# Optimization experiments

Measured on AMD Instinct MI355X. Metric: run time of the kernel, lower is better.

Reference implementation:

```python
import jax, jax.numpy as jnp
import numpy as np

N_NODES = 100000
N_EDGES = 1600000
D_FEAT = 64
HIDDEN = 64


def _glorot(key, shape):
    fan_in, fan_out = shape[1], shape[0]
    limit = float(np.sqrt(6.0 / (fan_in + fan_out)))
    return jax.random.uniform(key, shape, jnp.float32, -limit, limit)


def setup_inputs() -> dict:
    key = jax.random.key(0)
    ks = jax.random.split(key, 8)
    x = jax.random.normal(ks[0], (N_NODES, D_FEAT), jnp.float32)
    edge_index = jax.random.randint(ks[1], (2, N_EDGES), 0, N_NODES, jnp.int64)
    # SAGEConv params: lin_l applied to aggregated neighbors (has bias),
    # lin_r applied to root/self features (no bias in PyG default).
    params = {
        "W1_l": _glorot(ks[2], (HIDDEN, D_FEAT)),
        "b1": jnp.zeros((HIDDEN,), jnp.float32),
        "W1_r": _glorot(ks[3], (HIDDEN, D_FEAT)),
        "W2_l": _glorot(ks[4], (HIDDEN, HIDDEN)),
        "b2": jnp.zeros((HIDDEN,), jnp.float32),
        "W2_r": _glorot(ks[5], (HIDDEN, HIDDEN)),
    }
    return {"x": x, "edge_index": edge_index, **params}


def _sage_conv(x, src, dst, deg_inv, W_l, b, W_r):
    # mean-aggregate neighbor features: gather at src, segment-sum at dst
    msg = jax.ops.segment_sum(x[src], dst, num_segments=N_NODES)  # [N, F]
    agg = msg * deg_inv[:, None]
    return agg @ W_l.T + b + x @ W_r.T


def reference(x, edge_index, W1_l, b1, W1_r, W2_l, b2, W2_r):
    src, dst = edge_index[0], edge_index[1]
    deg = jax.ops.segment_sum(jnp.ones((N_EDGES,), x.dtype), dst,
                              num_segments=N_NODES)
    deg_inv = 1.0 / jnp.maximum(deg, 1.0)  # PyG mean clamps count to >=1
    h = jax.nn.relu(_sage_conv(x, src, dst, deg_inv, W1_l, b1, W1_r))
    out = _sage_conv(h, src, dst, deg_inv, W2_l, b2, W2_r)
    return out
```

## Files before the change

kernel.cpp:

```cpp
#include <hip/hip_runtime.h>
#include <hip/hip_bf16.h>

#define FEAT 64

typedef __bf16 bf16x8 __attribute__((ext_vector_type(8)));
typedef __bf16 bf16x4 __attribute__((ext_vector_type(4)));
typedef float  f32x4  __attribute__((ext_vector_type(4)));

__global__ __launch_bounds__(256)
void zero1_kernel(int* __restrict__ a, int n) {
    int i = blockIdx.x * 256 + threadIdx.x;
    if (i < n) a[i] = 0;
}

__global__ __launch_bounds__(256)
void zero2_kernel(int* __restrict__ a, int* __restrict__ b, int n) {
    int i = blockIdx.x * 256 + threadIdx.x;
    if (i < n) { a[i] = 0; b[i] = 0; }
}

__global__ void detect_idx_kernel(const unsigned* __restrict__ w, int* __restrict__ flag) {
    __shared__ int any_nz;
    if (threadIdx.x == 0) any_nz = 0;
    __syncthreads();
    if (w[2 * threadIdx.x + 1] != 0u) atomicOr(&any_nz, 1);
    __syncthreads();
    if (threadIdx.x == 0) *flag = (any_nz == 0) ? 1 : 0;
}

__device__ __forceinline__ int load_idx_clamped(const void* ei, long long i, int is64, int n_nodes) {
    int v = is64 ? (int)((const long long*)ei)[i] : ((const int*)ei)[i];
    v = v < 0 ? 0 : v;
    return v >= n_nodes ? n_nodes - 1 : v;
}


__global__ __launch_bounds__(256)
void bucket_count_kernel(const void* __restrict__ ei, const int* __restrict__ flagp,
                         int* __restrict__ gcnt, int n_edges, int n_nodes) {
    __shared__ int cnt[512];
    const int t = threadIdx.x;
    cnt[t] = 0; cnt[t + 256] = 0;
    __syncthreads();
    const int is64 = *flagp;
    for (int e = blockIdx.x * 256 + t; e < n_edges; e += gridDim.x * 256) {
        int d = load_idx_clamped(ei, (long long)n_edges + e, is64, n_nodes);
        atomicAdd(&cnt[d >> 9], 1);
    }
    __syncthreads();
    if (cnt[t])       atomicAdd(&gcnt[t], cnt[t]);
    if (cnt[t + 256]) atomicAdd(&gcnt[t + 256], cnt[t + 256]);
}

__global__ void bucket_scan_kernel(const int* __restrict__ gcnt, int* __restrict__ gbase,
                                   int* __restrict__ gcur, int n_edges) {
    __shared__ int sh[512];
    int t = threadIdx.x;
    int v = gcnt[t];
    sh[t] = v;
    __syncthreads();
    for (int off = 1; off < 512; off <<= 1) {
        int u = (t >= off) ? sh[t - off] : 0;
        __syncthreads();
        sh[t] += u;
        __syncthreads();
    }
    int excl = sh[t] - v;
    gbase[t] = excl;
    gcur[t]  = excl;
    if (t == 511) gbase[512] = n_edges;
}

__global__ __launch_bounds__(256)
void multisplit_kernel(const void* __restrict__ ei, const int* __restrict__ flagp,
                       int* __restrict__ gcur, unsigned* __restrict__ B,
                       int n_edges, int n_nodes) {
    __shared__ unsigned sv[4096];
    __shared__ unsigned dv[4096];
    __shared__ int cnt[512];
    __shared__ int cur[512];
    const int t = threadIdx.x;
    const int is64 = *flagp;
    const int ntiles = (n_edges + 4095) >> 12;
    for (int tile = blockIdx.x; tile < ntiles; tile += gridDim.x) {
        cnt[t] = 0; cnt[t + 256] = 0;
        __syncthreads();
        #pragma unroll
        for (int k = 0; k < 16; ++k) {
            int i = k * 256 + t;
            int e = (tile << 12) + i;
            unsigned dmark = 0xFFFFFFFFu, s = 0;
            if (e < n_edges) {
                s     = (unsigned)load_idx_clamped(ei, e, is64, n_nodes);
                int d = load_idx_clamped(ei, (long long)n_edges + e, is64, n_nodes);
                dmark = (unsigned)d;
                atomicAdd(&cnt[d >> 9], 1);
            }
            sv[i] = s; dv[i] = dmark;
        }
        __syncthreads();
        if (cnt[t])       cur[t]       = atomicAdd(&gcur[t], cnt[t]);
        if (cnt[t + 256]) cur[t + 256] = atomicAdd(&gcur[t + 256], cnt[t + 256]);
        __syncthreads();
        #pragma unroll
        for (int k = 0; k < 16; ++k) {
            int i = k * 256 + t;
            unsigned d = dv[i];
            if (d != 0xFFFFFFFFu) {
                int pos = atomicAdd(&cur[d >> 9], 1);
                pos = pos < 0 ? 0 : (pos >= n_edges ? n_edges - 1 : pos);
                B[pos] = ((d & 511u) << 17) | sv[i];
            }
        }
        __syncthreads();
    }
}

__global__ __launch_bounds__(256)
void csr_build2_kernel(const unsigned* __restrict__ B, const int* __restrict__ gbase,
                       int* __restrict__ degc, int* __restrict__ offs,
                       float* __restrict__ dinv, int* __restrict__ csr,
                       int n_edges, int n_nodes) {
    __shared__ int cnt[512];
    __shared__ int scn[512];
    __shared__ int cur[512];
    const int b = blockIdx.x, t = threadIdx.x;
    cnt[t] = 0; cnt[t + 256] = 0;
    __syncthreads();
    const int lo = gbase[b], hi = gbase[b + 1];
    for (int i = lo + t; i < hi; i += 256) {
        unsigned v = B[i];
        atomicAdd(&cnt[v >> 17], 1);
    }
    __syncthreads();
    scn[t] = cnt[t]; scn[t + 256] = cnt[t + 256];
    __syncthreads();
    for (int off = 1; off < 512; off <<= 1) {
        int u0 = (t >= off) ? scn[t - off] : 0;
        int u1 = (t + 256 >= off) ? scn[t + 256 - off] : 0;
        __syncthreads();
        scn[t] += u0; scn[t + 256] += u1;
        __syncthreads();
    }
    const int base = gbase[b];
    int e0 = base + scn[t] - cnt[t];
    int e1 = base + scn[t + 256] - cnt[t + 256];
    cur[t] = e0; cur[t + 256] = e1;
    int n0 = b * 512 + t, n1 = n0 + 256;
    if (n0 < n_nodes) {
        degc[n0] = cnt[t]; offs[n0] = e0;
        dinv[n0] = 1.0f / fmaxf((float)cnt[t], 1.0f);
    }
    if (n1 < n_nodes) {
        degc[n1] = cnt[t + 256]; offs[n1] = e1;
        dinv[n1] = 1.0f / fmaxf((float)cnt[t + 256], 1.0f);
    }
    __syncthreads();
    for (int i = lo + t; i < hi; i += 256) {
        unsigned v = B[i];
        int pos = atomicAdd(&cur[v >> 17], 1);
        pos = pos < 0 ? 0 : (pos >= n_edges ? n_edges - 1 : pos);
        csr[pos] = (int)(v & 0x1FFFFu);
    }
}

__global__ __launch_bounds__(256)
void scan_partial_kernel(const int* __restrict__ degc, int* __restrict__ part, int n_nodes) {
    __shared__ int sh[256];
    int i = blockIdx.x * 256 + threadIdx.x;
    sh[threadIdx.x] = (i < n_nodes) ? degc[i] : 0;
    __syncthreads();
    for (int off = 128; off > 0; off >>= 1) {
        if (threadIdx.x < off) sh[threadIdx.x] += sh[threadIdx.x + off];
        __syncthreads();
    }
    if (threadIdx.x == 0) part[blockIdx.x] = sh[0];
}

__global__ void scan_top_kernel(int* __restrict__ part, int nparts) {
    __shared__ int sh[512];
    int t = threadIdx.x;
    int v = (t < nparts) ? part[t] : 0;
    sh[t] = v;
    __syncthreads();
    for (int off = 1; off < 512; off <<= 1) {
        int u = (t >= off) ? sh[t - off] : 0;
        __syncthreads();
        sh[t] += u;
        __syncthreads();
    }
    if (t < nparts) part[t] = sh[t] - v;
}

__global__ __launch_bounds__(256)
void scan_final_kernel(const int* __restrict__ degc, const int* __restrict__ part,
                       int* __restrict__ offs, float* __restrict__ deg_inv, int n_nodes) {
    __shared__ int sh[256];
    int t = threadIdx.x;
    int i = blockIdx.x * 256 + t;
    int v = (i < n_nodes) ? degc[i] : 0;
    sh[t] = v;
    __syncthreads();
    for (int off = 1; off < 256; off <<= 1) {
        int u = (t >= off) ? sh[t - off] : 0;
        __syncthreads();
        sh[t] += u;
        __syncthreads();
    }
    if (i < n_nodes) {
        offs[i]    = sh[t] - v + part[blockIdx.x];
        deg_inv[i] = 1.0f / fmaxf((float)v, 1.0f);
    }
}

__global__ __launch_bounds__(256)
void hist_kernel(const void* __restrict__ ei, const int* __restrict__ flagp,
                 int* __restrict__ degc, int n_edges, int n_nodes) {
    int e = blockIdx.x * 256 + threadIdx.x;
    if (e >= n_edges) return;
    int d = load_idx_clamped(ei, (long long)n_edges + e, *flagp, n_nodes);
    atomicAdd(&degc[d], 1);
}

__global__ __launch_bounds__(256)
void csr_scatter_kernel(const void* __restrict__ ei, const int* __restrict__ flagp,
                        const int* __restrict__ offs, int* __restrict__ cursor,
                        int* __restrict__ csr, int n_edges, int n_nodes) {
    int e = blockIdx.x * 256 + threadIdx.x;
    if (e >= n_edges) return;
    int is64 = *flagp;
    int s = load_idx_clamped(ei, e, is64, n_nodes);
    int d = load_idx_clamped(ei, (long long)n_edges + e, is64, n_nodes);
    int pos = offs[d] + atomicAdd(&cursor[d], 1);
    pos = pos < 0 ? 0 : (pos >= n_edges ? n_edges - 1 : pos);
    csr[pos] = s;
}

__global__ __launch_bounds__(256)
void cast_w_kernel(const float* __restrict__ a, const float* __restrict__ b,
                   const float* __restrict__ c, const float* __restrict__ d,
                   __bf16* __restrict__ o) {
    int i = blockIdx.x * 256 + threadIdx.x;
    if (i < FEAT * FEAT) {
        o[i]         = (__bf16)a[i];
        o[4096 + i]  = (__bf16)b[i];
        o[8192 + i]  = (__bf16)c[i];
        o[12288 + i] = (__bf16)d[i];
    }
}

__global__ __launch_bounds__(256)
void cast_x_kernel(const float* __restrict__ x, __bf16* __restrict__ xb, int n4) {
    int i = blockIdx.x * 256 + threadIdx.x;
    if (i < n4) {
        float4 v = ((const float4*)x)[i];
        bf16x4 o;
        o.x = (__bf16)v.x; o.y = (__bf16)v.y; o.z = (__bf16)v.z; o.w = (__bf16)v.w;
        ((bf16x4*)xb)[i] = o;
    }
}

__global__ __launch_bounds__(256)
void gather_bf16_kernel(const __bf16* __restrict__ hin, const int* __restrict__ offs,
                        const int* __restrict__ degc, const float* __restrict__ dinv,
                        const int* __restrict__ csr, __bf16* __restrict__ agg,
                        int n_nodes) {
    const int t = threadIdx.x, lane = t & 63, g = lane >> 4, u = lane & 15;
    const int gw = blockIdx.x * 4 + (t >> 6), nw = gridDim.x * 4;
    for (int n = gw; n < n_nodes; n += nw) {
        int rs = offs[n], cnt = degc[n];
        float a0 = 0.f, a1 = 0.f, a2 = 0.f, a3 = 0.f;
        for (int c = 0; c < cnt; c += 64) {
            int chunk = min(64, cnt - c);
            int myid = (lane < chunk) ? (int)__builtin_nontemporal_load(&csr[rs + c + lane]) : 0;
            myid = myid < 0 ? 0 : (myid >= n_nodes ? n_nodes - 1 : myid);
            for (int q = 0; q < chunk; q += 16) {
                int q0 = q + g, q1 = q + g + 4, q2 = q + g + 8, q3 = q + g + 12;
                int s0 = __shfl(myid, q0);
                int s1 = __shfl(myid, q1);
                int s2 = __shfl(myid, q2);
                int s3 = __shfl(myid, q3);
                float m0 = (q0 < chunk) ? 1.f : 0.f;
                float m1 = (q1 < chunk) ? 1.f : 0.f;
                float m2 = (q2 < chunk) ? 1.f : 0.f;
                float m3 = (q3 < chunk) ? 1.f : 0.f;
                bf16x4 v0 = ((const bf16x4*)hin)[(size_t)s0 * 16 + u];
                bf16x4 v1 = ((const bf16x4*)hin)[(size_t)s1 * 16 + u];
                bf16x4 v2 = ((const bf16x4*)hin)[(size_t)s2 * 16 + u];
                bf16x4 v3 = ((const bf16x4*)hin)[(size_t)s3 * 16 + u];
                a0 = fmaf(m0, (float)v0.x, a0); a1 = fmaf(m0, (float)v0.y, a1);
                a2 = fmaf(m0, (float)v0.z, a2); a3 = fmaf(m0, (float)v0.w, a3);
                a0 = fmaf(m1, (float)v1.x, a0); a1 = fmaf(m1, (float)v1.y, a1);
                a2 = fmaf(m1, (float)v1.z, a2); a3 = fmaf(m1, (float)v1.w, a3);
                a0 = fmaf(m2, (float)v2.x, a0); a1 = fmaf(m2, (float)v2.y, a1);
                a2 = fmaf(m2, (float)v2.z, a2); a3 = fmaf(m2, (float)v2.w, a3);
                a0 = fmaf(m3, (float)v3.x, a0); a1 = fmaf(m3, (float)v3.y, a1);
                a2 = fmaf(m3, (float)v3.z, a2); a3 = fmaf(m3, (float)v3.w, a3);
            }
        }
        a0 += __shfl_xor(a0, 16); a1 += __shfl_xor(a1, 16);
        a2 += __shfl_xor(a2, 16); a3 += __shfl_xor(a3, 16);
        a0 += __shfl_xor(a0, 32); a1 += __shfl_xor(a1, 32);
        a2 += __shfl_xor(a2, 32); a3 += __shfl_xor(a3, 32);
        if (g == 0) {
            float di = dinv[n];
            bf16x4 o;
            o.x = (__bf16)(a0 * di); o.y = (__bf16)(a1 * di);
            o.z = (__bf16)(a2 * di); o.w = (__bf16)(a3 * di);
            ((bf16x4*)agg)[(size_t)n * 16 + u] = o;
        }
    }
}

__global__ __launch_bounds__(256)
void gather_f32_kernel(const float* __restrict__ xin, const int* __restrict__ offs,
                       const int* __restrict__ degc, const float* __restrict__ dinv,
                       const int* __restrict__ csr, __bf16* __restrict__ agg,
                       int n_nodes) {
    const int t = threadIdx.x, lane = t & 63, g = lane >> 4, u = lane & 15;
    const int gw = blockIdx.x * 4 + (t >> 6), nw = gridDim.x * 4;
    for (int n = gw; n < n_nodes; n += nw) {
        int rs = offs[n], cnt = degc[n];
        float a0 = 0.f, a1 = 0.f, a2 = 0.f, a3 = 0.f;
        for (int c = 0; c < cnt; c += 64) {
            int chunk = min(64, cnt - c);
            int myid = (lane < chunk) ? (int)__builtin_nontemporal_load(&csr[rs + c + lane]) : 0;
            myid = myid < 0 ? 0 : (myid >= n_nodes ? n_nodes - 1 : myid);
            for (int q = 0; q < chunk; q += 16) {
                int q0 = q + g, q1 = q + g + 4, q2 = q + g + 8, q3 = q + g + 12;
                int s0 = __shfl(myid, q0), s1 = __shfl(myid, q1);
                int s2 = __shfl(myid, q2), s3 = __shfl(myid, q3);
                float m0 = (q0 < chunk) ? 1.f : 0.f;
                float m1 = (q1 < chunk) ? 1.f : 0.f;
                float m2 = (q2 < chunk) ? 1.f : 0.f;
                float m3 = (q3 < chunk) ? 1.f : 0.f;
                float4 v0 = ((const float4*)xin)[(size_t)s0 * 16 + u];
                float4 v1 = ((const float4*)xin)[(size_t)s1 * 16 + u];
                float4 v2 = ((const float4*)xin)[(size_t)s2 * 16 + u];
                float4 v3 = ((const float4*)xin)[(size_t)s3 * 16 + u];
                a0 = fmaf(m0, v0.x, a0); a1 = fmaf(m0, v0.y, a1);
                a2 = fmaf(m0, v0.z, a2); a3 = fmaf(m0, v0.w, a3);
                a0 = fmaf(m1, v1.x, a0); a1 = fmaf(m1, v1.y, a1);
                a2 = fmaf(m1, v1.z, a2); a3 = fmaf(m1, v1.w, a3);
                a0 = fmaf(m2, v2.x, a0); a1 = fmaf(m2, v2.y, a1);
                a2 = fmaf(m2, v2.z, a2); a3 = fmaf(m2, v2.w, a3);
                a0 = fmaf(m3, v3.x, a0); a1 = fmaf(m3, v3.y, a1);
                a2 = fmaf(m3, v3.z, a2); a3 = fmaf(m3, v3.w, a3);
            }
        }
        a0 += __shfl_xor(a0, 16); a1 += __shfl_xor(a1, 16);
        a2 += __shfl_xor(a2, 16); a3 += __shfl_xor(a3, 16);
        a0 += __shfl_xor(a0, 32); a1 += __shfl_xor(a1, 32);
        a2 += __shfl_xor(a2, 32); a3 += __shfl_xor(a3, 32);
        if (g == 0) {
            float di = dinv[n];
            bf16x4 o;
            o.x = (__bf16)(a0 * di); o.y = (__bf16)(a1 * di);
            o.z = (__bf16)(a2 * di); o.w = (__bf16)(a3 * di);
            ((bf16x4*)agg)[(size_t)n * 16 + u] = o;
        }
    }
}

__global__ __launch_bounds__(256)
void gemm_l1b_kernel(const __bf16* __restrict__ Ag, const __bf16* __restrict__ xb,
                     const __bf16* __restrict__ Bl, const __bf16* __restrict__ Br,
                     const float* __restrict__ bias,
                     __bf16* __restrict__ hout, int n_nodes) {
    const int t = threadIdx.x, lane = t & 63;
    const int quad = lane >> 4, r16 = lane & 15;
    bf16x8 bl[2][4], br[2][4];
    #pragma unroll
    for (int ks = 0; ks < 2; ++ks)
        #pragma unroll
        for (int ct = 0; ct < 4; ++ct) {
            int f = ct * 16 + r16, k = ks * 32 + quad * 8;
            bl[ks][ct] = *(const bf16x8*)(Bl + f * 64 + k);
            br[ks][ct] = *(const bf16x8*)(Br + f * 64 + k);
        }
    const int m0 = (blockIdx.x * 4 + (t >> 6)) * 16;
    if (m0 >= n_nodes) return;
    int mrow = m0 + r16; if (mrow >= n_nodes) mrow = n_nodes - 1;
    bf16x8 ag[2], ax[2];
    #pragma unroll
    for (int ks = 0; ks < 2; ++ks) {
        ag[ks] = *(const bf16x8*)(Ag + (size_t)mrow * 64 + ks * 32 + quad * 8);
        ax[ks] = *(const bf16x8*)(xb + (size_t)mrow * 64 + ks * 32 + quad * 8);
    }
    #pragma unroll
    for (int ct = 0; ct < 4; ++ct) {
        f32x4 acc = {0.f, 0.f, 0.f, 0.f};
        acc = __builtin_amdgcn_mfma_f32_16x16x32_bf16(ag[0], bl[0][ct], acc, 0, 0, 0);
        acc = __builtin_amdgcn_mfma_f32_16x16x32_bf16(ag[1], bl[1][ct], acc, 0, 0, 0);
        acc = __builtin_amdgcn_mfma_f32_16x16x32_bf16(ax[0], br[0][ct], acc, 0, 0, 0);
        acc = __builtin_amdgcn_mfma_f32_16x16x32_bf16(ax[1], br[1][ct], acc, 0, 0, 0);
        int col = ct * 16 + r16;
        float bv = bias[col];
        #pragma unroll
        for (int rg = 0; rg < 4; ++rg) {
            int n = m0 + quad * 4 + rg;
            if (n < n_nodes) {
                float o = acc[rg] + bv;
                hout[(size_t)n * 64 + col] = (__bf16)fmaxf(o, 0.f);
            }
        }
    }
}

__global__ __launch_bounds__(256)
void gemm_l1_kernel(const __bf16* __restrict__ Ag, const float* __restrict__ xin,
                    const __bf16* __restrict__ Bl, const __bf16* __restrict__ Br,
                    const float* __restrict__ bias,
                    __bf16* __restrict__ hout, int n_nodes) {
    const int t = threadIdx.x, lane = t & 63;
    const int quad = lane >> 4, r16 = lane & 15;
    bf16x8 bl[2][4], br[2][4];
    #pragma unroll
    for (int ks = 0; ks < 2; ++ks)
        #pragma unroll
        for (int ct = 0; ct < 4; ++ct) {
            int f = ct * 16 + r16, k = ks * 32 + quad * 8;
            bl[ks][ct] = *(const bf16x8*)(Bl + f * 64 + k);
            br[ks][ct] = *(const bf16x8*)(Br + f * 64 + k);
        }
    const int m0 = (blockIdx.x * 4 + (t >> 6)) * 16;
    if (m0 >= n_nodes) return;
    int mrow = m0 + r16; if (mrow >= n_nodes) mrow = n_nodes - 1;
    bf16x8 ag[2], ax[2];
    #pragma unroll
    for (int ks = 0; ks < 2; ++ks) {
        ag[ks] = *(const bf16x8*)(Ag + (size_t)mrow * 64 + ks * 32 + quad * 8);
        const float* xr = xin + (size_t)mrow * 64 + ks * 32 + quad * 8;
        float4 p = *(const float4*)xr;
        float4 q = *(const float4*)(xr + 4);
        union { bf16x8 v; __bf16 e[8]; } U;
        U.e[0] = (__bf16)p.x; U.e[1] = (__bf16)p.y; U.e[2] = (__bf16)p.z; U.e[3] = (__bf16)p.w;
        U.e[4] = (__bf16)q.x; U.e[5] = (__bf16)q.y; U.e[6] = (__bf16)q.z; U.e[7] = (__bf16)q.w;
        ax[ks] = U.v;
    }
    #pragma unroll
    for (int ct = 0; ct < 4; ++ct) {
        f32x4 acc = {0.f, 0.f, 0.f, 0.f};
        acc = __builtin_amdgcn_mfma_f32_16x16x32_bf16(ag[0], bl[0][ct], acc, 0, 0, 0);
        acc = __builtin_amdgcn_mfma_f32_16x16x32_bf16(ag[1], bl[1][ct], acc, 0, 0, 0);
        acc = __builtin_amdgcn_mfma_f32_16x16x32_bf16(ax[0], br[0][ct], acc, 0, 0, 0);
        acc = __builtin_amdgcn_mfma_f32_16x16x32_bf16(ax[1], br[1][ct], acc, 0, 0, 0);
        int col = ct * 16 + r16;
        float bv = bias[col];
        #pragma unroll
        for (int rg = 0; rg < 4; ++rg) {
            int n = m0 + quad * 4 + rg;
            if (n < n_nodes) {
                float o = acc[rg] + bv;
                hout[(size_t)n * 64 + col] = (__bf16)fmaxf(o, 0.f);
            }
        }
    }
}

__global__ __launch_bounds__(256)
void gemm_l2_kernel(const __bf16* __restrict__ Ag, const __bf16* __restrict__ Ah,
                    const __bf16* __restrict__ Bl, const __bf16* __restrict__ Br,
                    const float* __restrict__ bias,
                    float* __restrict__ out, int n_nodes) {
    const int t = threadIdx.x, lane = t & 63;
    const int quad = lane >> 4, r16 = lane & 15;
    bf16x8 bl[2][4], br[2][4];
    #pragma unroll
    for (int ks = 0; ks < 2; ++ks)
        #pragma unroll
        for (int ct = 0; ct < 4; ++ct) {
            int f = ct * 16 + r16, k = ks * 32 + quad * 8;
            bl[ks][ct] = *(const bf16x8*)(Bl + f * 64 + k);
            br[ks][ct] = *(const bf16x8*)(Br + f * 64 + k);
        }
    const int m0 = (blockIdx.x * 4 + (t >> 6)) * 16;
    if (m0 >= n_nodes) return;
    int mrow = m0 + r16; if (mrow >= n_nodes) mrow = n_nodes - 1;
    bf16x8 ag[2], ah[2];
    #pragma unroll
    for (int ks = 0; ks < 2; ++ks) {
        ag[ks] = *(const bf16x8*)(Ag + (size_t)mrow * 64 + ks * 32 + quad * 8);
        ah[ks] = *(const bf16x8*)(Ah + (size_t)mrow * 64 + ks * 32 + quad * 8);
    }
    #pragma unroll
    for (int ct = 0; ct < 4; ++ct) {
        f32x4 acc = {0.f, 0.f, 0.f, 0.f};
        acc = __builtin_amdgcn_mfma_f32_16x16x32_bf16(ag[0], bl[0][ct], acc, 0, 0, 0);
        acc = __builtin_amdgcn_mfma_f32_16x16x32_bf16(ag[1], bl[1][ct], acc, 0, 0, 0);
        acc = __builtin_amdgcn_mfma_f32_16x16x32_bf16(ah[0], br[0][ct], acc, 0, 0, 0);
        acc = __builtin_amdgcn_mfma_f32_16x16x32_bf16(ah[1], br[1][ct], acc, 0, 0, 0);
        int col = ct * 16 + r16;
        float bv = bias[col];
        #pragma unroll
        for (int rg = 0; rg < 4; ++rg) {
            int n = m0 + quad * 4 + rg;
            if (n < n_nodes) out[(size_t)n * 64 + col] = acc[rg] + bv;
        }
    }
}

__global__ __launch_bounds__(256)
void sage_fused_l1_kernel(const float* __restrict__ xin,
                          const int* __restrict__ offs, const int* __restrict__ degc,
                          const float* __restrict__ deg_inv, const int* __restrict__ csr,
                          const float* __restrict__ Wl, const float* __restrict__ bias,
                          const float* __restrict__ Wr,
                          __bf16* __restrict__ hout, int n_nodes) {
    __shared__ float WlT[FEAT * 65], WrT[FEAT * 65], bsh[FEAT];
    __shared__ float aggS[4][FEAT], selfS[4][FEAT];
    const int t = threadIdx.x;
    #pragma unroll
    for (int p = 0; p < 16; ++p) {
        int i = t + p * 256, j = i >> 6, k = i & 63;
        WlT[k * 65 + j] = Wl[i];
        WrT[k * 65 + j] = Wr[i];
    }
    if (t < FEAT) bsh[t] = bias[t];
    __syncthreads();
    const int w = t >> 6, f = t & 63;
    const int n_groups = (n_nodes + 3) >> 2;
    for (int g = blockIdx.x; g < n_groups; g += gridDim.x) {
        int n = g * 4 + w;
        bool act = (n < n_nodes);
        if (act) {
            int rs = offs[n], cnt = degc[n];
            float acc = 0.f;
            for (int c = 0; c < cnt; c += 64) {
                int chunk = min(64, cnt - c);
                int myid = (f < chunk) ? csr[rs + c + f] : 0;
                #pragma unroll 4
                for (int q = 0; q < chunk; ++q) {
                    int s = __shfl(myid, q);
                    acc += xin[(long long)s * FEAT + f];
                }
            }
            aggS[w][f]  = acc * deg_inv[n];
            selfS[w][f] = xin[(long long)n * FEAT + f];
        }
        __syncthreads();
        if (act) {
            float o = bsh[f];
            #pragma unroll
            for (int k = 0; k < FEAT; ++k) {
                o = fmaf(aggS[w][k],  WlT[k * 65 + f], o);
                o = fmaf(selfS[w][k], WrT[k * 65 + f], o);
            }
            o = fmaxf(o, 0.f);
            hout[(long long)n * FEAT + f] = (__bf16)o;
        }
        __syncthreads();
    }
}

__global__ __launch_bounds__(256)
void sage_fused_l2_kernel(const __bf16* __restrict__ hin,
                          const int* __restrict__ offs, const int* __restrict__ degc,
                          const float* __restrict__ deg_inv, const int* __restrict__ csr,
                          const float* __restrict__ Wl, const float* __restrict__ bias,
                          const float* __restrict__ Wr,
                          float* __restrict__ out, int n_nodes) {
    __shared__ float WlT[FEAT * 65], WrT[FEAT * 65], bsh[FEAT];
    __shared__ float aggS[4][FEAT], selfS[4][FEAT];
    const int t = threadIdx.x;
    #pragma unroll
    for (int p = 0; p < 16; ++p) {
        int i = t + p * 256, j = i >> 6, k = i & 63;
        WlT[k * 65 + j] = Wl[i];
        WrT[k * 65 + j] = Wr[i];
    }
    if (t < FEAT) bsh[t] = bias[t];
    __syncthreads();
    const int w = t >> 6, f = t & 63;
    const int n_groups = (n_nodes + 3) >> 2;
    for (int g = blockIdx.x; g < n_groups; g += gridDim.x) {
        int n = g * 4 + w;
        bool act = (n < n_nodes);
        if (act) {
            int rs = offs[n], cnt = degc[n];
            float acc = 0.f;
            for (int c = 0; c < cnt; c += 64) {
                int chunk = min(64, cnt - c);
                int myid = (f < chunk) ? csr[rs + c + f] : 0;
                #pragma unroll 4
                for (int q = 0; q < chunk; ++q) {
                    int s = __shfl(myid, q);
                    acc += (float)hin[(long long)s * FEAT + f];
                }
            }
            aggS[w][f]  = acc * deg_inv[n];
            selfS[w][f] = (float)hin[(long long)n * FEAT + f];
        }
        __syncthreads();
        if (act) {
            float o = bsh[f];
            #pragma unroll
            for (int k = 0; k < FEAT; ++k) {
                o = fmaf(aggS[w][k],  WlT[k * 65 + f], o);
                o = fmaf(selfS[w][k], WrT[k * 65 + f], o);
            }
            out[(long long)n * FEAT + f] = o;
        }
        __syncthreads();
    }
}

extern "C" void kernel_launch(void* const* d_in, const int* in_sizes, int n_in,
                              void* d_out, int out_size, void* d_ws, size_t ws_size,
                              hipStream_t stream) {
    const float* x   = (const float*)d_in[0];
    const void*  ei  = d_in[1];
    const float* W1l = (const float*)d_in[2];
    const float* b1  = (const float*)d_in[3];
    const float* W1r = (const float*)d_in[4];
    const float* W2l = (const float*)d_in[5];
    const float* b2  = (const float*)d_in[6];
    const float* W2r = (const float*)d_in[7];
    float* out = (float*)d_out;

    const int n_nodes = in_sizes[0] / FEAT;
    const int n_edges = in_sizes[1] / 2;
    const int nparts  = (n_nodes + 255) / 256;
    const int egrid   = (n_edges + 255) / 256;
    const int NB      = (n_nodes + 511) >> 9;

    char* ws = (char*)d_ws;
    auto al = [](size_t v) { return (v + 255) & ~(size_t)255; };

    size_t o = 0;
    int*      flag  = (int*)(ws + o);      o += 256;
    int*      degc  = (int*)(ws + o);      o += al((size_t)n_nodes * 4);
    float*    dinv  = (float*)(ws + o);    o += al((size_t)n_nodes * 4);
    int*      offs  = (int*)(ws + o);      o += al((size_t)n_nodes * 4);
    int*      gcnt  = (int*)(ws + o);      o += al(512 * 4);
    int*      gbase = (int*)(ws + o);      o += al(513 * 4);
    int*      gcur  = (int*)(ws + o);      o += al(512 * 4);
    unsigned* B     = (unsigned*)(ws + o); o += al((size_t)n_edges * 4);
    int*      csr   = (int*)(ws + o);      o += al((size_t)n_edges * 4);
    __bf16*   xb    = (__bf16*)(ws + o);   o += al((size_t)n_nodes * FEAT * 2);
    __bf16*   wb    = (__bf16*)(ws + o);   o += al((size_t)4 * FEAT * FEAT * 2);
    __bf16*   agg   = (__bf16*)(ws + o);   o += al((size_t)n_nodes * FEAT * 2);
    __bf16*   h     = (__bf16*)(ws + o);   o += al((size_t)n_nodes * FEAT * 2);
    const size_t needT1 = o;

    size_t o3 = 0;
    int*    flag3   = (int*)(ws + o3);    o3 += 256;
    int*    degc3   = (int*)(ws + o3);    o3 += al((size_t)n_nodes * 4);
    float*  dinv3   = (float*)(ws + o3);  o3 += al((size_t)n_nodes * 4);
    int*    offs3   = (int*)(ws + o3);    o3 += al((size_t)n_nodes * 4);
    int*    cursor3 = (int*)(ws + o3);    o3 += al((size_t)n_nodes * 4);
    int*    part3   = (int*)(ws + o3);    o3 += al(2048);
    int*    csr3    = (int*)(ws + o3);    o3 += al((size_t)n_edges * 4);
    const size_t commonEnd3 = o3;
    __bf16* wb3  = (__bf16*)(ws + o3);    o3 += al((size_t)4 * FEAT * FEAT * 2);
    __bf16* agg3 = (__bf16*)(ws + o3);    o3 += al((size_t)n_nodes * FEAT * 2);
    __bf16* h3   = (__bf16*)(ws + o3);    o3 += al((size_t)n_nodes * FEAT * 2);
    const size_t needT3 = o3;

    const int n4 = n_nodes * FEAT / 4;
    const int mgrid = (n_nodes + 63) / 64;
    const int ggrid = 2048;
    const int ntiles = (n_edges + 4095) >> 12;

    if (ws_size >= needT1 && n_nodes <= 131072) {
        zero1_kernel<<<2, 256, 0, stream>>>(gcnt, 512);
        detect_idx_kernel<<<1, 256, 0, stream>>>((const unsigned*)ei, flag);
        bucket_count_kernel<<<512, 256, 0, stream>>>(ei, flag, gcnt, n_edges, n_nodes);
        bucket_scan_kernel<<<1, 512, 0, stream>>>(gcnt, gbase, gcur, n_edges);
        multisplit_kernel<<<ntiles, 256, 0, stream>>>(ei, flag, gcur, B, n_edges, n_nodes);
        cast_x_kernel<<<(n4 + 255) / 256, 256, 0, stream>>>(x, xb, n4);
        cast_w_kernel<<<16, 256, 0, stream>>>(W1l, W1r, W2l, W2r, wb);
        csr_build2_kernel<<<NB, 256, 0, stream>>>(B, gbase, degc, offs, dinv, csr, n_edges, n_nodes);
        gather_bf16_kernel<<<ggrid, 256, 0, stream>>>(xb, offs, degc, dinv, csr, agg, n_nodes);
        gemm_l1b_kernel<<<mgrid, 256, 0, stream>>>(agg, xb, wb, wb + 4096, b1, h, n_nodes);
        gather_bf16_kernel<<<ggrid, 256, 0, stream>>>(h, offs, degc, dinv, csr, agg, n_nodes);
        gemm_l2_kernel<<<mgrid, 256, 0, stream>>>(agg, h, wb + 8192, wb + 12288, b2, out, n_nodes);
    } else if (ws_size >= needT3) {
        zero2_kernel<<<nparts, 256, 0, stream>>>(degc3, cursor3, n_nodes);
        detect_idx_kernel<<<1, 256, 0, stream>>>((const unsigned*)ei, flag3);
        hist_kernel<<<egrid, 256, 0, stream>>>(ei, flag3, degc3, n_edges, n_nodes);
        scan_partial_kernel<<<nparts, 256, 0, stream>>>(degc3, part3, n_nodes);
        scan_top_kernel<<<1, 512, 0, stream>>>(part3, nparts);
        scan_final_kernel<<<nparts, 256, 0, stream>>>(degc3, part3, offs3, dinv3, n_nodes);
        csr_scatter_kernel<<<egrid, 256, 0, stream>>>(ei, flag3, offs3, cursor3, csr3, n_edges, n_nodes);
        cast_w_kernel<<<16, 256, 0, stream>>>(W1l, W1r, W2l, W2r, wb3);
        gather_f32_kernel<<<ggrid, 256, 0, stream>>>(x, offs3, degc3, dinv3, csr3, agg3, n_nodes);
        gemm_l1_kernel<<<mgrid, 256, 0, stream>>>(agg3, x, wb3, wb3 + 4096, b1, h3, n_nodes);
        gather_bf16_kernel<<<ggrid, 256, 0, stream>>>(h3, offs3, degc3, dinv3, csr3, agg3, n_nodes);
        gemm_l2_kernel<<<mgrid, 256, 0, stream>>>(agg3, h3, wb3 + 8192, wb3 + 12288, b2, out, n_nodes);
    } else {
        __bf16* hf = (__bf16*)(ws + commonEnd3);
        zero2_kernel<<<nparts, 256, 0, stream>>>(degc3, cursor3, n_nodes);
        detect_idx_kernel<<<1, 256, 0, stream>>>((const unsigned*)ei, flag3);
        hist_kernel<<<egrid, 256, 0, stream>>>(ei, flag3, degc3, n_edges, n_nodes);
        scan_partial_kernel<<<nparts, 256, 0, stream>>>(degc3, part3, n_nodes);
        scan_top_kernel<<<1, 512, 0, stream>>>(part3, nparts);
        scan_final_kernel<<<nparts, 256, 0, stream>>>(degc3, part3, offs3, dinv3, n_nodes);
        csr_scatter_kernel<<<egrid, 256, 0, stream>>>(ei, flag3, offs3, cursor3, csr3, n_edges, n_nodes);
        const int n_groups = (n_nodes + 3) / 4;
        const int fgrid = n_groups < 4096 ? n_groups : 4096;
        sage_fused_l1_kernel<<<fgrid, 256, 0, stream>>>(x, offs3, degc3, dinv3, csr3,
                                                        W1l, b1, W1r, hf, n_nodes);
        sage_fused_l2_kernel<<<fgrid, 256, 0, stream>>>(hf, offs3, degc3, dinv3, csr3,
                                                        W2l, b2, W2r, out, n_nodes);
    }
}
```

Baseline: 280.7 us.

## Prefetch next node's CSR metadata in bf16 gather, fold zeroing into detect kernel

The bf16 gather kernel now software-pipelines across its grid-stride loop. It loads the next node's offset, degree, inverse degree and first chunk of neighbor ids while the current node is being accumulated, to hide the dependent-load latency at the start of each node. The separate zero kernel is removed and the bucket-count zeroing moves into detect_idx_kernel, saving one launch. Int64 index loads now read only the low 32-bit word, which halves the load width but assumes non-negative indices below 2^31.

```diff
diff --git a/kernel.cpp b/kernel.cpp
--- a/kernel.cpp
+++ b/kernel.cpp
@@ -8,28 +8,25 @@
 typedef float  f32x4  __attribute__((ext_vector_type(4)));
 
 __global__ __launch_bounds__(256)
-void zero1_kernel(int* __restrict__ a, int n) {
-    int i = blockIdx.x * 256 + threadIdx.x;
-    if (i < n) a[i] = 0;
-}
-
-__global__ __launch_bounds__(256)
 void zero2_kernel(int* __restrict__ a, int* __restrict__ b, int n) {
     int i = blockIdx.x * 256 + threadIdx.x;
     if (i < n) { a[i] = 0; b[i] = 0; }
 }
 
-__global__ void detect_idx_kernel(const unsigned* __restrict__ w, int* __restrict__ flag) {
+__global__ void detect_idx_kernel(const unsigned* __restrict__ w, int* __restrict__ flag,
+                                  int* __restrict__ zcnt) {
     __shared__ int any_nz;
     if (threadIdx.x == 0) any_nz = 0;
     __syncthreads();
     if (w[2 * threadIdx.x + 1] != 0u) atomicOr(&any_nz, 1);
+    zcnt[threadIdx.x] = 0;
+    zcnt[threadIdx.x + 256] = 0;
     __syncthreads();
     if (threadIdx.x == 0) *flag = (any_nz == 0) ? 1 : 0;
 }
 
 __device__ __forceinline__ int load_idx_clamped(const void* ei, long long i, int is64, int n_nodes) {
-    int v = is64 ? (int)((const long long*)ei)[i] : ((const int*)ei)[i];
+    int v = is64 ? ((const int*)ei)[2 * i] : ((const int*)ei)[i];
     v = v < 0 ? 0 : v;
     return v >= n_nodes ? n_nodes - 1 : v;
 }
@@ -267,12 +264,21 @@
                         int n_nodes) {
     const int t = threadIdx.x, lane = t & 63, g = lane >> 4, u = lane & 15;
     const int gw = blockIdx.x * 4 + (t >> 6), nw = gridDim.x * 4;
+    if (gw >= n_nodes) return;
+    int rs = offs[gw], cnt = degc[gw];
+    float di = dinv[gw];
+    int lim0 = cnt < 64 ? cnt : 64;
+    int pf = (lane < lim0) ? (int)__builtin_nontemporal_load(&csr[rs + lane]) : 0;
     for (int n = gw; n < n_nodes; n += nw) {
-        int rs = offs[n], cnt = degc[n];
+        const int nn = n + nw;
+        int rs2 = 0, cnt2 = 0;
+        float di2 = 1.0f;
+        if (nn < n_nodes) { rs2 = offs[nn]; cnt2 = degc[nn]; di2 = dinv[nn]; }
         float a0 = 0.f, a1 = 0.f, a2 = 0.f, a3 = 0.f;
-        for (int c = 0; c < cnt; c += 64) {
-            int chunk = min(64, cnt - c);
-            int myid = (lane < chunk) ? (int)__builtin_nontemporal_load(&csr[rs + c + lane]) : 0;
+        int myid = pf;
+        int c = 0;
+        while (true) {
+            int chunk = cnt - c; chunk = chunk > 64 ? 64 : chunk;
             myid = myid < 0 ? 0 : (myid >= n_nodes ? n_nodes - 1 : myid);
             for (int q = 0; q < chunk; q += 16) {
                 int q0 = q + g, q1 = q + g + 4, q2 = q + g + 8, q3 = q + g + 12;
@@ -297,18 +303,27 @@
                 a0 = fmaf(m3, (float)v3.x, a0); a1 = fmaf(m3, (float)v3.y, a1);
                 a2 = fmaf(m3, (float)v3.z, a2); a3 = fmaf(m3, (float)v3.w, a3);
             }
+            c += 64;
+            if (c >= cnt) break;
+            int rem = cnt - c, lim = rem < 64 ? rem : 64;
+            myid = (lane < lim) ? (int)__builtin_nontemporal_load(&csr[rs + c + lane]) : 0;
+        }
+        {
+            int lim2 = cnt2 < 64 ? cnt2 : 64;
+            pf = (nn < n_nodes && lane < lim2)
+                     ? (int)__builtin_nontemporal_load(&csr[rs2 + lane]) : 0;
         }
         a0 += __shfl_xor(a0, 16); a1 += __shfl_xor(a1, 16);
         a2 += __shfl_xor(a2, 16); a3 += __shfl_xor(a3, 16);
         a0 += __shfl_xor(a0, 32); a1 += __shfl_xor(a1, 32);
         a2 += __shfl_xor(a2, 32); a3 += __shfl_xor(a3, 32);
         if (g == 0) {
-            float di = dinv[n];
             bf16x4 o;
             o.x = (__bf16)(a0 * di); o.y = (__bf16)(a1 * di);
             o.z = (__bf16)(a2 * di); o.w = (__bf16)(a3 * di);
             ((bf16x4*)agg)[(size_t)n * 16 + u] = o;
         }
+        rs = rs2; cnt = cnt2; di = di2;
     }
 }
 
@@ -663,8 +678,7 @@
     const int ntiles = (n_edges + 4095) >> 12;
 
     if (ws_size >= needT1 && n_nodes <= 131072) {
-        zero1_kernel<<<2, 256, 0, stream>>>(gcnt, 512);
-        detect_idx_kernel<<<1, 256, 0, stream>>>((const unsigned*)ei, flag);
+        detect_idx_kernel<<<1, 256, 0, stream>>>((const unsigned*)ei, flag, gcnt);
         bucket_count_kernel<<<512, 256, 0, stream>>>(ei, flag, gcnt, n_edges, n_nodes);
         bucket_scan_kernel<<<1, 512, 0, stream>>>(gcnt, gbase, gcur, n_edges);
         multisplit_kernel<<<ntiles, 256, 0, stream>>>(ei, flag, gcur, B, n_edges, n_nodes);
@@ -677,7 +691,7 @@
         gemm_l2_kernel<<<mgrid, 256, 0, stream>>>(agg, h, wb + 8192, wb + 12288, b2, out, n_nodes);
     } else if (ws_size >= needT3) {
         zero2_kernel<<<nparts, 256, 0, stream>>>(degc3, cursor3, n_nodes);
-        detect_idx_kernel<<<1, 256, 0, stream>>>((const unsigned*)ei, flag3);
+        detect_idx_kernel<<<1, 256, 0, stream>>>((const unsigned*)ei, flag3, part3);
         hist_kernel<<<egrid, 256, 0, stream>>>(ei, flag3, degc3, n_edges, n_nodes);
         scan_partial_kernel<<<nparts, 256, 0, stream>>>(degc3, part3, n_nodes);
         scan_top_kernel<<<1, 512, 0, stream>>>(part3, nparts);
@@ -691,7 +705,7 @@
     } else {
         __bf16* hf = (__bf16*)(ws + commonEnd3);
         zero2_kernel<<<nparts, 256, 0, stream>>>(degc3, cursor3, n_nodes);
-        detect_idx_kernel<<<1, 256, 0, stream>>>((const unsigned*)ei, flag3);
+        detect_idx_kernel<<<1, 256, 0, stream>>>((const unsigned*)ei, flag3, part3);
         hist_kernel<<<egrid, 256, 0, stream>>>(ei, flag3, degc3, n_edges, n_nodes);
         scan_partial_kernel<<<nparts, 256, 0, stream>>>(degc3, part3, n_nodes);
         scan_top_kernel<<<1, 512, 0, stream>>>(part3, nparts);
```

After: 266.5 us. 5.1% less time.
